# Kernel tuning notes

Hardware: AMD Instinct MI355X
Metric: run time of the kernel (lower is better)

The kernel has to match this reference:

```python
import jax, jax.numpy as jnp
import numpy as np

ENERGY_PERCENT = 0.8


def setup_inputs() -> dict:
    key = jax.random.key(0)
    B, T, C = 32, 4096, 128
    x = jax.random.normal(key, (B, T, C), dtype=jnp.float32)
    return {"x": x}


def reference(x):
    # x: [B, T, C]; FFT along time axis.
    T = x.shape[1]
    xf = jnp.fft.rfft(x, axis=1)                      # [B, F, C] complex
    energies = jnp.abs(xf) ** 2                       # [B, F, C]

    # Sort energies descending along freq axis (per batch, per channel).
    sorted_indices = jnp.argsort(-energies, axis=1)   # [B, F, C] int
    sorted_energies = jnp.take_along_axis(energies, sorted_indices, axis=1)

    total_energy = jnp.sum(energies, axis=1, keepdims=True)        # [B, 1, C]
    cumulative = jnp.cumsum(sorted_energies, axis=1)               # [B, F, C]

    # Smallest k such that cumulative energy exceeds energy_percent of total.
    exceeded = cumulative > total_energy * ENERGY_PERCENT          # [B, F, C] bool
    k = jnp.argmax(exceeded, axis=1) + 1                           # [B, C]

    # rank[b, f, c] = position of frequency f in the descending energy order;
    # this is the inverse permutation of sorted_indices (argsort of a permutation).
    rank = jnp.argsort(sorted_indices, axis=1)                     # [B, F, C]

    is_low_freq = rank < k[:, None, :]                             # [B, F, C]

    # Zero out the high-energy ("low-frequency") components -> residual x_var.
    mask = jnp.where(is_low_freq, 0.0, 1.0).astype(x.dtype)        # [B, F, C]
    x_var = jnp.fft.irfft(xf * mask, n=T, axis=1)                  # [B, T, C]
    x_inv = x - x_var
    return (x_var, x_inv)
```

## Files before the change

### kernel.cpp

```cpp
#include <hip/hip_runtime.h>


#define TLEN 4096
#define N2   2048
#define CCH  128
#define BB   32
#define NSER (BB * CCH)
#define HALF 16777216

#define LP(i) ((i) + ((i) >> 5))

__device__ __forceinline__ void dft4(float vr[4], float vi[4], float s) {
  float t0r = vr[0] + vr[2], t0i = vi[0] + vi[2];
  float t1r = vr[0] - vr[2], t1i = vi[0] - vi[2];
  float t2r = vr[1] + vr[3], t2i = vi[1] + vi[3];
  float d3r = vr[1] - vr[3], d3i = vi[1] - vi[3];
  float t3r = -s * d3i, t3i = s * d3r;
  vr[0] = t0r + t2r; vi[0] = t0i + t2i;
  vr[1] = t1r + t3r; vi[1] = t1i + t3i;
  vr[2] = t0r - t2r; vi[2] = t0i - t2i;
  vr[3] = t1r - t3r; vi[3] = t1i - t3i;
}

__device__ __forceinline__ void dft8(float vr[8], float vi[8], float s) {
  float er[4]  = {vr[0], vr[2], vr[4], vr[6]};
  float ei[4]  = {vi[0], vi[2], vi[4], vi[6]};
  float odr[4] = {vr[1], vr[3], vr[5], vr[7]};
  float odi[4] = {vi[1], vi[3], vi[5], vi[7]};
  dft4(er, ei, s);
  dft4(odr, odi, s);
  const float c = 0.70710678118654752440f;
  float wr[4] = {1.0f, c, 0.0f, -c};
  float wi[4] = {0.0f, s * c, s, s * c};
  #pragma unroll
  for (int k = 0; k < 4; ++k) {
    float tr = wr[k] * odr[k] - wi[k] * odi[k];
    float ti = wr[k] * odi[k] + wi[k] * odr[k];
    vr[k]     = er[k] + tr; vi[k]     = ei[k] + ti;
    vr[k + 4] = er[k] - tr; vi[k + 4] = ei[k] - ti;
  }
}

__device__ __forceinline__ void stage8(float* zr, float* zi, int tid, int Ns, float s) {
  int j = tid;
  int p = j & (Ns - 1);
  float ang0 = s * 6.28318530717958647692f * (float)p / (float)(Ns * 8);
  float vr[8], vi[8];
  #pragma unroll
  for (int r = 0; r < 8; ++r) {
    int idx = LP(j + (r << 8));
    float ar = zr[idx], ai = zi[idx];
    float sn, cs;
    __sincosf(ang0 * (float)r, &sn, &cs);
    vr[r] = ar * cs - ai * sn;
    vi[r] = ar * sn + ai * cs;
  }
  dft8(vr, vi, s);
  __syncthreads();
  int idxD = ((j - p) << 3) + p;
  #pragma unroll
  for (int r = 0; r < 8; ++r) {
    int idx = LP(idxD + r * Ns);
    zr[idx] = vr[r]; zi[idx] = vi[r];
  }
  __syncthreads();
}

__device__ __forceinline__ void stage4_last(float* zr, float* zi, int tid, float s) {
  #pragma unroll
  for (int half = 0; half < 2; ++half) {
    int j = tid + (half << 8);
    float ang0 = s * 6.28318530717958647692f * (float)j / 2048.0f;
    float vr[4], vi[4];
    #pragma unroll
    for (int r = 0; r < 4; ++r) {
      int idx = LP(j + (r << 9));
      float ar = zr[idx], ai = zi[idx];
      float sn, cs;
      __sincosf(ang0 * (float)r, &sn, &cs);
      vr[r] = ar * cs - ai * sn;
      vi[r] = ar * sn + ai * cs;
    }
    dft4(vr, vi, s);
    #pragma unroll
    for (int r = 0; r < 4; ++r) {
      int idx = LP(j + (r << 9));
      zr[idx] = vr[r]; zi[idx] = vi[r];
    }
  }
  __syncthreads();
}

__device__ __forceinline__ void fft2048(float* zr, float* zi, int tid, float s) {
  stage8(zr, zi, tid, 1, s);
  stage8(zr, zi, tid, 8, s);
  stage8(zr, zi, tid, 64, s);
  stage4_last(zr, zi, tid, s);
}

__device__ __forceinline__ double block_sum(double v, double* red, int tid) {
  #pragma unroll
  for (int o = 32; o > 0; o >>= 1) v += __shfl_down(v, o, 64);
  if ((tid & 63) == 0) red[tid >> 6] = v;
  __syncthreads();
  double t = red[0] + red[1] + red[2] + red[3];
  __syncthreads();
  return t;
}

__global__ __launch_bounds__(256) void fourier_filter_series(float* __restrict__ buf) {
  __shared__ float zr[2112], zi[2112];
  __shared__ float Xr[2113], Xi[2113];
  __shared__ double red[4];
  int tid = threadIdx.x;
  float* p = buf + (size_t)blockIdx.x * TLEN;

  const float2* p2 = (const float2*)p;
  for (int k = tid; k < N2; k += 256) {
    float2 v = p2[k];
    zr[LP(k)] = v.x; zi[LP(k)] = v.y;
  }
  __syncthreads();

  fft2048(zr, zi, tid, -1.0f);

  for (int k = tid; k <= 1024; k += 256) {
    int mk = (N2 - k) & (N2 - 1);
    float akr = zr[LP(k)],  aki = zi[LP(k)];
    float bkr = zr[LP(mk)], bki = zi[LP(mk)];
    float Er  = 0.5f * (akr + bkr);
    float Ei  = 0.5f * (aki - bki);
    float Or_ = 0.5f * (aki + bki);
    float Oi  = 0.5f * (bkr - akr);
    float sn, cs;
    __sincosf(-3.14159265358979323846f * (float)k / 2048.0f, &sn, &cs);
    float tr = cs * Or_ - sn * Oi;
    float ti = cs * Oi + sn * Or_;
    Xr[LP(k)] = Er + tr;         Xi[LP(k)] = Ei + ti;
    Xr[LP(N2 - k)] = Er - tr;    Xi[LP(N2 - k)] = -(Ei - ti);
  }
  __syncthreads();

  float eb[9];
  double tloc = 0.0;
  #pragma unroll
  for (int jj = 0; jj < 9; ++jj) {
    int k = tid + (jj << 8);
    if (k <= N2) {
      float xr = Xr[LP(k)], xi = Xi[LP(k)];
      eb[jj] = xr * xr + xi * xi;
      tloc += (double)eb[jj];
    } else {
      eb[jj] = -1.0f;
    }
  }
  double total = block_sum(tloc, red, tid);
  double thresh = 0.8 * total;

  unsigned lo = 0u, hi = 0x7F7FFFFFu;
  for (int it = 0; it < 31; ++it) {
    unsigned mid = (unsigned)(((unsigned long long)lo + (unsigned long long)hi + 1ull) >> 1);
    float tau = __uint_as_float(mid);
    double loc = 0.0;
    #pragma unroll
    for (int jj = 0; jj < 9; ++jj)
      if (eb[jj] >= tau) loc += (double)eb[jj];
    double ssum = block_sum(loc, red, tid);
    if (ssum > thresh) lo = mid; else hi = mid - 1;
  }
  float tau = __uint_as_float(lo);

  for (int k = tid; k < N2; k += 256) {
    int mk = N2 - k;
    float xkr = Xr[LP(k)],  xki = Xi[LP(k)];
    float xmr = Xr[LP(mk)], xmi = Xi[LP(mk)];
    float ek = xkr * xkr + xki * xki;
    float em = xmr * xmr + xmi * xmi;
    if (ek >= tau) { xkr = 0.0f; xki = 0.0f; }
    if (em >= tau) { xmr = 0.0f; xmi = 0.0f; }
    float Er = 0.5f * (xkr + xmr);
    float Ei = 0.5f * (xki - xmi);
    float Br = 0.5f * (xkr - xmr);
    float Bi = 0.5f * (xki + xmi);
    float sn, cs;
    __sincosf(3.14159265358979323846f * (float)k / 2048.0f, &sn, &cs);
    float Or_ = cs * Br - sn * Bi;
    float Oi  = cs * Bi + sn * Br;
    zr[LP(k)] = Er - Oi;
    zi[LP(k)] = Ei + Or_;
  }
  __syncthreads();

  fft2048(zr, zi, tid, 1.0f);

  const float scale = 1.0f / 2048.0f;
  float2* po = (float2*)p;
  for (int k = tid; k < N2; k += 256) {
    float2 v;
    v.x = zr[LP(k)] * scale;
    v.y = zi[LP(k)] * scale;
    po[k] = v;
  }
}

__global__ __launch_bounds__(256) void transpose_fwd(const float* __restrict__ x, float* __restrict__ xT) {
  __shared__ float tile[32][33];
  int t0 = blockIdx.x << 5, c0 = blockIdx.y << 5, b = blockIdx.z;
  int col = threadIdx.x & 31, r0 = threadIdx.x >> 5;
  const float* xp = x + ((size_t)b * TLEN + t0) * CCH + c0;
  #pragma unroll
  for (int r = 0; r < 32; r += 8) tile[r + r0][col] = xp[(size_t)(r + r0) * CCH + col];
  __syncthreads();
  float* tp = xT + ((size_t)b * CCH + c0) * TLEN + t0;
  #pragma unroll
  for (int r = 0; r < 32; r += 8) tp[(size_t)(r + r0) * TLEN + col] = tile[col][r + r0];
}

__global__ __launch_bounds__(256) void finalize_t(const float* __restrict__ xvT, const float* __restrict__ x,
                                                  float* __restrict__ xvar, float* __restrict__ xinv) {
  __shared__ float tile[32][33];
  int t0 = blockIdx.x << 5, c0 = blockIdx.y << 5, b = blockIdx.z;
  int col = threadIdx.x & 31, r0 = threadIdx.x >> 5;
  const float* sp = xvT + ((size_t)b * CCH + c0) * TLEN + t0;
  #pragma unroll
  for (int r = 0; r < 32; r += 8) tile[r + r0][col] = sp[(size_t)(r + r0) * TLEN + col];
  __syncthreads();
  size_t base = ((size_t)b * TLEN + t0) * CCH + c0;
  #pragma unroll
  for (int r = 0; r < 32; r += 8) {
    size_t off = base + (size_t)(r + r0) * CCH + col;
    float v = tile[col][r + r0];
    float xv = x[off];
    xvar[off] = v;
    xinv[off] = xv - v;
  }
}

__global__ __launch_bounds__(256) void transpose_back(const float* __restrict__ xvT, float* __restrict__ xvar) {
  __shared__ float tile[32][33];
  int t0 = blockIdx.x << 5, c0 = blockIdx.y << 5, b = blockIdx.z;
  int col = threadIdx.x & 31, r0 = threadIdx.x >> 5;
  const float* sp = xvT + ((size_t)b * CCH + c0) * TLEN + t0;
  #pragma unroll
  for (int r = 0; r < 32; r += 8) tile[r + r0][col] = sp[(size_t)(r + r0) * TLEN + col];
  __syncthreads();
  size_t base = ((size_t)b * TLEN + t0) * CCH + c0;
  #pragma unroll
  for (int r = 0; r < 32; r += 8) xvar[base + (size_t)(r + r0) * CCH + col] = tile[col][r + r0];
}

__global__ __launch_bounds__(256) void sub_kernel(const float4* __restrict__ x, const float4* __restrict__ xv,
                                                  float4* __restrict__ xi, int n4) {
  int i = blockIdx.x * 256 + threadIdx.x;
  if (i < n4) {
    float4 a = x[i], b = xv[i];
    xi[i] = make_float4(a.x - b.x, a.y - b.y, a.z - b.z, a.w - b.w);
  }
}

extern "C" void kernel_launch(void* const* d_in, const int* in_sizes, int n_in,
                              void* d_out, int out_size, void* d_ws, size_t ws_size,
                              hipStream_t stream) {
  const float* x = (const float*)d_in[0];
  float* out  = (float*)d_out;
  float* xvar = out;
  float* xinv = out + HALF;

  bool use_ws = ws_size >= (size_t)NSER * TLEN * sizeof(float);
  float* buf = use_ws ? (float*)d_ws : xinv;

  dim3 tgrid(TLEN / 32, CCH / 32, BB);
  transpose_fwd<<<tgrid, 256, 0, stream>>>(x, buf);
  fourier_filter_series<<<NSER, 256, 0, stream>>>(buf);
  if (use_ws) {
    finalize_t<<<tgrid, 256, 0, stream>>>(buf, x, xvar, xinv);
  } else {
    transpose_back<<<tgrid, 256, 0, stream>>>(buf, xvar);
    sub_kernel<<<(HALF / 4 + 255) / 256, 256, 0, stream>>>((const float4*)x, (const float4*)xvar,
                                                           (float4*)xinv, HALF / 4);
  }
}
```

Before: 346.3 us.

## Cut FFT twiddle trig, drop double reductions, fuse spectrum buffers, widen transposes

The FFT stages now compute one sincos per thread and derive the higher twiddles by complex multiplication, and the first radix-8 stage skips twiddles entirely. The real-to-complex post-processing keeps the spectrum in place, computes energies in registers, and advances twiddles by rotation. Binary-search reductions switch from double to float with double-buffered partials, which removes one barrier per iteration. The transpose kernels move to 64x64 tiles with float4 global accesses. Float accumulation and recurrence-based twiddles may lower accuracy and could flip threshold decisions near ties.

Result: faster. 303.3 us (-12.4%).

```diff
diff --git a/kernel.cpp b/kernel.cpp
--- a/kernel.cpp
+++ b/kernel.cpp
@@ -7,8 +7,15 @@
 #define BB   32
 #define NSER (BB * CCH)
 #define HALF 16777216
+#define PI_F 3.14159265358979323846f
 
 #define LP(i) ((i) + ((i) >> 5))
+
+__device__ __forceinline__ void cmul(float& r, float& i, float br, float bi) {
+  float tr = r * br - i * bi;
+  i = r * bi + i * br;
+  r = tr;
+}
 
 __device__ __forceinline__ void dft4(float vr[4], float vi[4], float s) {
   float t0r = vr[0] + vr[2], t0i = vi[0] + vi[2];
@@ -41,26 +48,54 @@
   }
 }
 
-__device__ __forceinline__ void stage8(float* zr, float* zi, int tid, int Ns, float s) {
+__device__ __forceinline__ void stage8_first(float* zr, float* zi, int tid, float s) {
+  float vr[8], vi[8];
+  #pragma unroll
+  for (int r = 0; r < 8; ++r) {
+    int idx = LP(tid + (r << 8));
+    vr[r] = zr[idx]; vi[r] = zi[idx];
+  }
+  dft8(vr, vi, s);
+  __syncthreads();
+  #pragma unroll
+  for (int r = 0; r < 8; ++r) {
+    int idx = LP((tid << 3) + r);
+    zr[idx] = vr[r]; zi[idx] = vi[r];
+  }
+  __syncthreads();
+}
+
+template <int NS>
+__device__ __forceinline__ void stage8_tw(float* zr, float* zi, int tid, float s) {
   int j = tid;
-  int p = j & (Ns - 1);
-  float ang0 = s * 6.28318530717958647692f * (float)p / (float)(Ns * 8);
+  int p = j & (NS - 1);
   float vr[8], vi[8];
   #pragma unroll
   for (int r = 0; r < 8; ++r) {
     int idx = LP(j + (r << 8));
-    float ar = zr[idx], ai = zi[idx];
-    float sn, cs;
-    __sincosf(ang0 * (float)r, &sn, &cs);
-    vr[r] = ar * cs - ai * sn;
-    vi[r] = ar * sn + ai * cs;
-  }
+    vr[r] = zr[idx]; vi[r] = zi[idx];
+  }
+  float ang = s * 6.28318530717958647692f * (float)p / (float)(NS * 8);
+  float s1, c1; __sincosf(ang, &s1, &c1);
+  float c2 = c1 * c1 - s1 * s1, s2 = 2.0f * c1 * s1;
+  float c3 = c2 * c1 - s2 * s1, s3 = c2 * s1 + s2 * c1;
+  float c4 = c2 * c2 - s2 * s2, s4 = 2.0f * c2 * s2;
+  float c5 = c4 * c1 - s4 * s1, s5 = c4 * s1 + s4 * c1;
+  float c6 = c4 * c2 - s4 * s2, s6 = c4 * s2 + s4 * c2;
+  float c7 = c4 * c3 - s4 * s3, s7 = c4 * s3 + s4 * c3;
+  cmul(vr[1], vi[1], c1, s1);
+  cmul(vr[2], vi[2], c2, s2);
+  cmul(vr[3], vi[3], c3, s3);
+  cmul(vr[4], vi[4], c4, s4);
+  cmul(vr[5], vi[5], c5, s5);
+  cmul(vr[6], vi[6], c6, s6);
+  cmul(vr[7], vi[7], c7, s7);
   dft8(vr, vi, s);
   __syncthreads();
   int idxD = ((j - p) << 3) + p;
   #pragma unroll
   for (int r = 0; r < 8; ++r) {
-    int idx = LP(idxD + r * Ns);
+    int idx = LP(idxD + r * NS);
     zr[idx] = vr[r]; zi[idx] = vi[r];
   }
   __syncthreads();
@@ -70,17 +105,19 @@
   #pragma unroll
   for (int half = 0; half < 2; ++half) {
     int j = tid + (half << 8);
-    float ang0 = s * 6.28318530717958647692f * (float)j / 2048.0f;
+    float ang = s * PI_F * (float)j * (1.0f / 1024.0f);
+    float s1, c1; __sincosf(ang, &s1, &c1);
+    float c2 = c1 * c1 - s1 * s1, s2 = 2.0f * c1 * s1;
+    float c3 = c2 * c1 - s2 * s1, s3 = c2 * s1 + s2 * c1;
     float vr[4], vi[4];
     #pragma unroll
     for (int r = 0; r < 4; ++r) {
       int idx = LP(j + (r << 9));
-      float ar = zr[idx], ai = zi[idx];
-      float sn, cs;
-      __sincosf(ang0 * (float)r, &sn, &cs);
-      vr[r] = ar * cs - ai * sn;
-      vi[r] = ar * sn + ai * cs;
+      vr[r] = zr[idx]; vi[r] = zi[idx];
     }
+    cmul(vr[1], vi[1], c1, s1);
+    cmul(vr[2], vi[2], c2, s2);
+    cmul(vr[3], vi[3], c3, s3);
     dft4(vr, vi, s);
     #pragma unroll
     for (int r = 0; r < 4; ++r) {
@@ -92,30 +129,29 @@
 }
 
 __device__ __forceinline__ void fft2048(float* zr, float* zi, int tid, float s) {
-  stage8(zr, zi, tid, 1, s);
-  stage8(zr, zi, tid, 8, s);
-  stage8(zr, zi, tid, 64, s);
+  stage8_first(zr, zi, tid, s);
+  stage8_tw<8>(zr, zi, tid, s);
+  stage8_tw<64>(zr, zi, tid, s);
   stage4_last(zr, zi, tid, s);
 }
 
-__device__ __forceinline__ double block_sum(double v, double* red, int tid) {
+__device__ __forceinline__ float block_sum(float v, float* red, int tid, int bank) {
   #pragma unroll
   for (int o = 32; o > 0; o >>= 1) v += __shfl_down(v, o, 64);
-  if ((tid & 63) == 0) red[tid >> 6] = v;
-  __syncthreads();
-  double t = red[0] + red[1] + red[2] + red[3];
-  __syncthreads();
-  return t;
+  if ((tid & 63) == 0) red[(bank << 2) + (tid >> 6)] = v;
+  __syncthreads();
+  int b4 = bank << 2;
+  return red[b4] + red[b4 + 1] + red[b4 + 2] + red[b4 + 3];
 }
 
 __global__ __launch_bounds__(256) void fourier_filter_series(float* __restrict__ buf) {
-  __shared__ float zr[2112], zi[2112];
-  __shared__ float Xr[2113], Xi[2113];
-  __shared__ double red[4];
+  __shared__ float zr[2113], zi[2113];
+  __shared__ float red[8];
   int tid = threadIdx.x;
   float* p = buf + (size_t)blockIdx.x * TLEN;
 
   const float2* p2 = (const float2*)p;
+  #pragma unroll
   for (int k = tid; k < N2; k += 256) {
     float2 v = p2[k];
     zr[LP(k)] = v.x; zi[LP(k)] = v.y;
@@ -124,70 +160,88 @@
 
   fft2048(zr, zi, tid, -1.0f);
 
-  for (int k = tid; k <= 1024; k += 256) {
-    int mk = (N2 - k) & (N2 - 1);
-    float akr = zr[LP(k)],  aki = zi[LP(k)];
-    float bkr = zr[LP(mk)], bki = zi[LP(mk)];
+  float eb[9];
+  eb[8] = 0.0f;
+  const float RC  = 0.92387953251128675613f;
+  const float RSn = -0.38268343236508977173f;
+  float ws, wc;
+  __sincosf(-PI_F * (float)tid * (1.0f / 2048.0f), &ws, &wc);
+  #pragma unroll
+  for (int jj = 0; jj < 4; ++jj) {
+    int k = tid + (jj << 8);
+    int mkz = (N2 - k) & (N2 - 1);
+    int ik = LP(k), im = LP(N2 - k);
+    float akr = zr[ik],      aki = zi[ik];
+    float bkr = zr[LP(mkz)], bki = zi[LP(mkz)];
     float Er  = 0.5f * (akr + bkr);
     float Ei  = 0.5f * (aki - bki);
     float Or_ = 0.5f * (aki + bki);
     float Oi  = 0.5f * (bkr - akr);
-    float sn, cs;
-    __sincosf(-3.14159265358979323846f * (float)k / 2048.0f, &sn, &cs);
-    float tr = cs * Or_ - sn * Oi;
-    float ti = cs * Oi + sn * Or_;
-    Xr[LP(k)] = Er + tr;         Xi[LP(k)] = Ei + ti;
-    Xr[LP(N2 - k)] = Er - tr;    Xi[LP(N2 - k)] = -(Ei - ti);
-  }
-  __syncthreads();
-
-  float eb[9];
-  double tloc = 0.0;
-  #pragma unroll
-  for (int jj = 0; jj < 9; ++jj) {
-    int k = tid + (jj << 8);
-    if (k <= N2) {
-      float xr = Xr[LP(k)], xi = Xi[LP(k)];
-      eb[jj] = xr * xr + xi * xi;
-      tloc += (double)eb[jj];
-    } else {
-      eb[jj] = -1.0f;
-    }
-  }
-  double total = block_sum(tloc, red, tid);
-  double thresh = 0.8 * total;
+    float tr = wc * Or_ - ws * Oi;
+    float ti = wc * Oi + ws * Or_;
+    float x0r = Er + tr, x0i = Ei + ti;
+    float x1r = Er - tr, x1i = ti - Ei;
+    zr[ik] = x0r; zi[ik] = x0i;
+    zr[im] = x1r; zi[im] = x1i;
+    eb[2 * jj]     = x0r * x0r + x0i * x0i;
+    eb[2 * jj + 1] = x1r * x1r + x1i * x1i;
+    float nwc = wc * RC - ws * RSn;
+    ws = wc * RSn + ws * RC; wc = nwc;
+  }
+  if (tid == 0) {
+    int i4 = LP(1024);
+    float re = zr[i4], im_ = zi[i4];
+    zi[i4] = -im_;
+    eb[8] = re * re + im_ * im_;
+  }
+
+  float tloc = 0.0f;
+  #pragma unroll
+  for (int s = 0; s < 9; ++s) tloc += eb[s];
+  float total = block_sum(tloc, red, tid, 0);
+  float thresh = 0.8f * total;
 
   unsigned lo = 0u, hi = 0x7F7FFFFFu;
   for (int it = 0; it < 31; ++it) {
-    unsigned mid = (unsigned)(((unsigned long long)lo + (unsigned long long)hi + 1ull) >> 1);
+    unsigned mid = (lo + hi + 1u) >> 1;
     float tau = __uint_as_float(mid);
-    double loc = 0.0;
+    float loc = 0.0f;
     #pragma unroll
-    for (int jj = 0; jj < 9; ++jj)
-      if (eb[jj] >= tau) loc += (double)eb[jj];
-    double ssum = block_sum(loc, red, tid);
+    for (int s = 0; s < 9; ++s) loc += (eb[s] >= tau) ? eb[s] : 0.0f;
+    float ssum = block_sum(loc, red, tid, (it + 1) & 1);
     if (ssum > thresh) lo = mid; else hi = mid - 1;
   }
   float tau = __uint_as_float(lo);
 
-  for (int k = tid; k < N2; k += 256) {
-    int mk = N2 - k;
-    float xkr = Xr[LP(k)],  xki = Xi[LP(k)];
-    float xmr = Xr[LP(mk)], xmi = Xi[LP(mk)];
-    float ek = xkr * xkr + xki * xki;
-    float em = xmr * xmr + xmi * xmi;
-    if (ek >= tau) { xkr = 0.0f; xki = 0.0f; }
-    if (em >= tau) { xmr = 0.0f; xmi = 0.0f; }
+  const float RSp = 0.38268343236508977173f;
+  __sincosf(PI_F * (float)tid * (1.0f / 2048.0f), &ws, &wc);
+  #pragma unroll
+  for (int jj = 0; jj < 4; ++jj) {
+    int k = tid + (jj << 8);
+    int ik = LP(k), im = LP(N2 - k);
+    float xkr = zr[ik], xki = zi[ik];
+    float xmr = zr[im], xmi = zi[im];
+    float ekk = xkr * xkr + xki * xki;
+    float emm = xmr * xmr + xmi * xmi;
+    if (ekk >= tau) { xkr = 0.0f; xki = 0.0f; }
+    if (emm >= tau) { xmr = 0.0f; xmi = 0.0f; }
     float Er = 0.5f * (xkr + xmr);
     float Ei = 0.5f * (xki - xmi);
     float Br = 0.5f * (xkr - xmr);
     float Bi = 0.5f * (xki + xmi);
-    float sn, cs;
-    __sincosf(3.14159265358979323846f * (float)k / 2048.0f, &sn, &cs);
-    float Or_ = cs * Br - sn * Bi;
-    float Oi  = cs * Bi + sn * Br;
-    zr[LP(k)] = Er - Oi;
-    zi[LP(k)] = Ei + Or_;
+    float Or_ = wc * Br - ws * Bi;
+    float Oi  = wc * Bi + ws * Br;
+    zr[ik] = Er - Oi;  zi[ik] = Ei + Or_;
+    zr[im] = Er + Oi;  zi[im] = Or_ - Ei;
+    float nwc = wc * RC - ws * RSp;
+    ws = wc * RSp + ws * RC; wc = nwc;
+  }
+  if (tid == 0) {
+    int i4 = LP(1024);
+    float re = zr[i4], im_ = zi[i4];
+    float e = re * re + im_ * im_;
+    if (e >= tau) { re = 0.0f; im_ = 0.0f; }
+    zr[i4] = re; zi[i4] = -im_;
   }
   __syncthreads();
 
@@ -195,6 +249,7 @@
 
   const float scale = 1.0f / 2048.0f;
   float2* po = (float2*)p;
+  #pragma unroll
   for (int k = tid; k < N2; k += 256) {
     float2 v;
     v.x = zr[LP(k)] * scale;
@@ -204,49 +259,79 @@
 }
 
 __global__ __launch_bounds__(256) void transpose_fwd(const float* __restrict__ x, float* __restrict__ xT) {
-  __shared__ float tile[32][33];
-  int t0 = blockIdx.x << 5, c0 = blockIdx.y << 5, b = blockIdx.z;
-  int col = threadIdx.x & 31, r0 = threadIdx.x >> 5;
-  const float* xp = x + ((size_t)b * TLEN + t0) * CCH + c0;
-  #pragma unroll
-  for (int r = 0; r < 32; r += 8) tile[r + r0][col] = xp[(size_t)(r + r0) * CCH + col];
-  __syncthreads();
-  float* tp = xT + ((size_t)b * CCH + c0) * TLEN + t0;
-  #pragma unroll
-  for (int r = 0; r < 32; r += 8) tp[(size_t)(r + r0) * TLEN + col] = tile[col][r + r0];
+  __shared__ float tile[64][65];
+  int t0 = blockIdx.x << 6, c0 = blockIdx.y << 6, b = blockIdx.z;
+  int m = threadIdx.x & 15, q = threadIdx.x >> 4;
+  #pragma unroll
+  for (int r = 0; r < 4; ++r) {
+    int t = q + (r << 4);
+    float4 v = *(const float4*)(x + ((size_t)b * TLEN + t0 + t) * CCH + c0 + (m << 2));
+    tile[t][(m << 2) + 0] = v.x; tile[t][(m << 2) + 1] = v.y;
+    tile[t][(m << 2) + 2] = v.z; tile[t][(m << 2) + 3] = v.w;
+  }
+  __syncthreads();
+  #pragma unroll
+  for (int r = 0; r < 4; ++r) {
+    int c = q + (r << 4);
+    int t4 = m << 2;
+    float4 v;
+    v.x = tile[t4 + 0][c]; v.y = tile[t4 + 1][c];
+    v.z = tile[t4 + 2][c]; v.w = tile[t4 + 3][c];
+    *(float4*)(xT + ((size_t)b * CCH + c0 + c) * TLEN + t0 + t4) = v;
+  }
 }
 
 __global__ __launch_bounds__(256) void finalize_t(const float* __restrict__ xvT, const float* __restrict__ x,
                                                   float* __restrict__ xvar, float* __restrict__ xinv) {
-  __shared__ float tile[32][33];
-  int t0 = blockIdx.x << 5, c0 = blockIdx.y << 5, b = blockIdx.z;
-  int col = threadIdx.x & 31, r0 = threadIdx.x >> 5;
-  const float* sp = xvT + ((size_t)b * CCH + c0) * TLEN + t0;
-  #pragma unroll
-  for (int r = 0; r < 32; r += 8) tile[r + r0][col] = sp[(size_t)(r + r0) * TLEN + col];
-  __syncthreads();
-  size_t base = ((size_t)b * TLEN + t0) * CCH + c0;
-  #pragma unroll
-  for (int r = 0; r < 32; r += 8) {
-    size_t off = base + (size_t)(r + r0) * CCH + col;
-    float v = tile[col][r + r0];
-    float xv = x[off];
-    xvar[off] = v;
-    xinv[off] = xv - v;
+  __shared__ float tile[64][65];
+  int t0 = blockIdx.x << 6, c0 = blockIdx.y << 6, b = blockIdx.z;
+  int m = threadIdx.x & 15, q = threadIdx.x >> 4;
+  #pragma unroll
+  for (int r = 0; r < 4; ++r) {
+    int c = q + (r << 4);
+    int t4 = m << 2;
+    float4 v = *(const float4*)(xvT + ((size_t)b * CCH + c0 + c) * TLEN + t0 + t4);
+    tile[t4 + 0][c] = v.x; tile[t4 + 1][c] = v.y;
+    tile[t4 + 2][c] = v.z; tile[t4 + 3][c] = v.w;
+  }
+  __syncthreads();
+  #pragma unroll
+  for (int r = 0; r < 4; ++r) {
+    int t = q + (r << 4);
+    int c4 = m << 2;
+    float4 v;
+    v.x = tile[t][c4 + 0]; v.y = tile[t][c4 + 1];
+    v.z = tile[t][c4 + 2]; v.w = tile[t][c4 + 3];
+    size_t off = ((size_t)b * TLEN + t0 + t) * CCH + c0 + c4;
+    float4 xv = *(const float4*)(x + off);
+    *(float4*)(xvar + off) = v;
+    *(float4*)(xinv + off) = make_float4(xv.x - v.x, xv.y - v.y, xv.z - v.z, xv.w - v.w);
   }
 }
 
 __global__ __launch_bounds__(256) void transpose_back(const float* __restrict__ xvT, float* __restrict__ xvar) {
-  __shared__ float tile[32][33];
-  int t0 = blockIdx.x << 5, c0 = blockIdx.y << 5, b = blockIdx.z;
-  int col = threadIdx.x & 31, r0 = threadIdx.x >> 5;
-  const float* sp = xvT + ((size_t)b * CCH + c0) * TLEN + t0;
-  #pragma unroll
-  for (int r = 0; r < 32; r += 8) tile[r + r0][col] = sp[(size_t)(r + r0) * TLEN + col];
-  __syncthreads();
-  size_t base = ((size_t)b * TLEN + t0) * CCH + c0;
-  #pragma unroll
-  for (int r = 0; r < 32; r += 8) xvar[base + (size_t)(r + r0) * CCH + col] = tile[col][r + r0];
+  __shared__ float tile[64][65];
+  int t0 = blockIdx.x << 6, c0 = blockIdx.y << 6, b = blockIdx.z;
+  int m = threadIdx.x & 15, q = threadIdx.x >> 4;
+  #pragma unroll
+  for (int r = 0; r < 4; ++r) {
+    int c = q + (r << 4);
+    int t4 = m << 2;
+    float4 v = *(const float4*)(xvT + ((size_t)b * CCH + c0 + c) * TLEN + t0 + t4);
+    tile[t4 + 0][c] = v.x; tile[t4 + 1][c] = v.y;
+    tile[t4 + 2][c] = v.z; tile[t4 + 3][c] = v.w;
+  }
+  __syncthreads();
+  #pragma unroll
+  for (int r = 0; r < 4; ++r) {
+    int t = q + (r << 4);
+    int c4 = m << 2;
+    float4 v;
+    v.x = tile[t][c4 + 0]; v.y = tile[t][c4 + 1];
+    v.z = tile[t][c4 + 2]; v.w = tile[t][c4 + 3];
+    size_t off = ((size_t)b * TLEN + t0 + t) * CCH + c0 + c4;
+    *(float4*)(xvar + off) = v;
+  }
 }
 
 __global__ __launch_bounds__(256) void sub_kernel(const float4* __restrict__ x, const float4* __restrict__ xv,
@@ -269,7 +354,7 @@
   bool use_ws = ws_size >= (size_t)NSER * TLEN * sizeof(float);
   float* buf = use_ws ? (float*)d_ws : xinv;
 
-  dim3 tgrid(TLEN / 32, CCH / 32, BB);
+  dim3 tgrid(TLEN / 64, CCH / 64, BB);
   transpose_fwd<<<tgrid, 256, 0, stream>>>(x, buf);
   fourier_filter_series<<<NSER, 256, 0, stream>>>(buf);
   if (use_ws) {
```
